# Optimization experiments

Hardware: AMD Instinct MI355X
Metric: run time of the kernel (lower is better)

The kernel has to match this reference:

```python
import jax, jax.numpy as jnp
import numpy as np

WS = 7          # window size (square)
HEADS = 16
LOGIT_MAX = float(np.log(1.0 / 0.01))


def _consts():
    # Continuous relative position bias coordinate table, Swin-v2 log-spaced.
    r = np.arange(-(WS - 1), WS)
    table = np.stack(np.meshgrid(r, r, indexing='ij'), axis=-1).astype(np.float32)  # [2W-1, 2W-1, 2]
    table = table / (WS - 1) * 8.0
    table = np.sign(table) * np.log2(np.abs(table) + 1.0) / np.log2(8.0)
    # Relative position index [N, N] into the flattened table.
    coords = np.stack(np.meshgrid(np.arange(WS), np.arange(WS), indexing='ij')).reshape(2, -1)
    rel = coords[:, :, None] - coords[:, None, :]
    idx = (rel[0] + WS - 1) * (2 * WS - 1) + (rel[1] + WS - 1)  # [49, 49]
    return table.reshape(-1, 2), idx.astype(np.int32)


def setup_inputs() -> dict:
    key = jax.random.key(0)
    ks = jax.random.split(key, 6)
    B, N, C = 2048, WS * WS, 512
    d = C // HEADS
    return {
        'x': jax.random.normal(ks[0], (B, N, C), jnp.float32),
        'w_qkv': jax.random.normal(ks[1], (C, 3 * C), jnp.float32) * (C ** -0.5),
        'q_bias': jnp.zeros((C,), jnp.float32),
        'v_bias': jnp.zeros((C,), jnp.float32),
        'logit_scale': jnp.full((HEADS, 1, 1), np.log(10.0), jnp.float32),
        'cpb_w1': jax.random.normal(ks[2], (2, 512), jnp.float32) * (2 ** -0.5),
        'cpb_b1': jnp.zeros((512,), jnp.float32),
        'cpb_w2': jax.random.normal(ks[3], (512, HEADS), jnp.float32) * (512 ** -0.5),
        'proj_w': jax.random.normal(ks[4], (C, C), jnp.float32) * (C ** -0.5),
        'proj_b': jnp.zeros((C,), jnp.float32),
    }


def _l2norm(x):
    # matches tf.math.l2_normalize (eps=1e-12 under a max)
    return x / jnp.sqrt(jnp.maximum(jnp.sum(x * x, axis=-1, keepdims=True), 1e-12))


def reference(x, w_qkv, q_bias, v_bias, logit_scale, cpb_w1, cpb_b1, cpb_w2, proj_w, proj_b):
    table, idx = _consts()
    table = jnp.asarray(table)   # [(2W-1)^2, 2]
    idx = jnp.asarray(idx)       # [N, N] int32 (constant)

    B, N, C = x.shape
    d = C // HEADS

    qkv = (x @ w_qkv).reshape(B, N, 3, HEADS, d).transpose(2, 0, 3, 1, 4)  # [3, B, H, N, d]
    q, k, v = qkv[0], qkv[1], qkv[2]
    q = q + q_bias.reshape(HEADS, 1, d)
    v = v + v_bias.reshape(HEADS, 1, d)

    # cosine attention with clamped learned logit scale
    attn = jnp.einsum('bhnd,bhmd->bhnm', _l2norm(q), _l2norm(k))
    scale = jnp.exp(jnp.minimum(logit_scale, LOGIT_MAX))  # [H,1,1]
    attn = attn * scale[None]

    # CPB MLP -> gather -> sigmoid bias
    bias_table = jax.nn.relu(table @ cpb_w1 + cpb_b1) @ cpb_w2          # [(2W-1)^2, H]
    bias = bias_table[idx.reshape(-1)].reshape(N, N, HEADS).transpose(2, 0, 1)  # [H, N, N]
    bias = 16.0 * jax.nn.sigmoid(bias)

    attn = jax.nn.softmax(attn + bias[None], axis=-1)

    out = jnp.einsum('bhnm,bhmd->bhnd', attn, v).transpose(0, 2, 1, 3).reshape(B, N, C)
    return out @ proj_w + proj_b
```

## Files before the change

### kernel.cpp

```cpp
#include <hip/hip_runtime.h>
#include <hip/hip_bf16.h>

typedef __bf16 bf16;
typedef __attribute__((ext_vector_type(8))) __bf16 bf16x8;
typedef __attribute__((ext_vector_type(4))) __bf16 bf16x4;
typedef __attribute__((ext_vector_type(4))) float floatx4;

#define HEADS 16
#define NTOK 49
#define MROWS (2048 * 49)
#define TILE_E 1568
#define LOGIT_MAX 4.6051702f


__device__ __forceinline__ void gload16(const void* g, void* l) {
  __builtin_amdgcn_global_load_lds((const __attribute__((address_space(1))) void*)g,
                                   (__attribute__((address_space(3))) void*)l, 16, 0, 0);
}


__global__ void cvt_x(const float* __restrict__ in, bf16* __restrict__ out, int n4) {
  int i = blockIdx.x * blockDim.x + threadIdx.x;
  const int stride = gridDim.x * blockDim.x;
  for (; i < n4; i += stride) {
    float4 v = ((const float4*)in)[i];
    bf16x4 o;
    o[0] = (bf16)v.x; o[1] = (bf16)v.y; o[2] = (bf16)v.z; o[3] = (bf16)v.w;
    *(bf16x4*)&out[(long)i * 4] = o;
  }
}

__global__ void transpose_bf16(const float* __restrict__ in, bf16* __restrict__ out,
                               int R, int C) {
  int idx = blockIdx.x * blockDim.x + threadIdx.x;
  if (idx < R * C) {
    int r = idx / C, c = idx % C;
    out[(long)c * R + r] = (bf16)in[(long)r * C + c];
  }
}


__global__ void cpb_mlp(const float* __restrict__ w1, const float* __restrict__ b1,
                        const float* __restrict__ w2, float* __restrict__ out169) {
  const int r = blockIdx.x;
  const int ti = r / 13, tj = r % 13;
  float v0 = (float)(ti - 6) * (8.0f / 6.0f);
  float v1 = (float)(tj - 6) * (8.0f / 6.0f);
  float s0 = (v0 > 0.f) ? 1.f : ((v0 < 0.f) ? -1.f : 0.f);
  float s1 = (v1 > 0.f) ? 1.f : ((v1 < 0.f) ? -1.f : 0.f);
  const float t0 = s0 * log2f(fabsf(v0) + 1.0f) * (1.0f / 3.0f);
  const float t1 = s1 * log2f(fabsf(v1) + 1.0f) * (1.0f / 3.0f);

  float acc[16];
#pragma unroll
  for (int h = 0; h < 16; ++h) acc[h] = 0.f;

  for (int c = threadIdx.x; c < 512; c += 64) {
    float hv = fmaxf(t0 * w1[c] + t1 * w1[512 + c] + b1[c], 0.f);
#pragma unroll
    for (int h = 0; h < 16; ++h) acc[h] += hv * w2[c * 16 + h];
  }
#pragma unroll
  for (int h = 0; h < 16; ++h) {
    float s = acc[h];
    for (int off = 32; off > 0; off >>= 1) s += __shfl_down(s, off);
    if (threadIdx.x == 0) out169[r * 16 + h] = s;
  }
}

__global__ void bias_expand(const float* __restrict__ out169, float* __restrict__ bias_sig) {
  int idx = blockIdx.x * blockDim.x + threadIdx.x;
  if (idx < 16 * 64 * 52) {
    int h = idx / 3328;
    int rem = idx % 3328;
    int q = rem / 52, k = rem % 52;
    float val = 0.f;
    if (q < 49 && k < 49) {
      int di = q / 7 - k / 7 + 6;
      int dj = q % 7 - k % 7 + 6;
      float v = out169[(di * 13 + dj) * 16 + h];
      val = 16.0f / (1.0f + expf(-v));
    }
    bias_sig[idx] = val;
  }
}


__device__ __forceinline__ void stage_tile(const bf16* __restrict__ G, int ldg,
                                           bf16* lds, int w, int lane) {
#pragma unroll
  for (int j = 0; j < 4; ++j) {
    const int rr = w * 32 + j * 8;
    const int row = rr + (lane >> 3);
    const int slot = (lane & 7) ^ (lane >> 3);
    gload16(G + (long)row * ldg + slot * 8, lds + rr * 64);
  }
}

template <int EPI>
__global__ __launch_bounds__(256, 4)
void gemm128(const bf16* __restrict__ A, const bf16* __restrict__ BT,
             void* __restrict__ Cout, const float* __restrict__ bias0,
             const float* __restrict__ bias1,
             bf16* __restrict__ Qp, bf16* __restrict__ Kp, bf16* __restrict__ Vp,
             int NT, int K, long N) {
  __shared__ bf16 AS[128][64];
  __shared__ bf16 BS[128][64];
  const int tid = threadIdx.x;
  const int lane = tid & 63, w = tid >> 6;
  const int l15 = lane & 15, g = lane >> 4;
  const int wm = w >> 1, wn = w & 1;

  int wg = blockIdx.x;
  wg = (wg & 7) * ((int)gridDim.x >> 3) + (wg >> 3);
  const long m0 = (long)(wg / NT) * 128;
  const long n0 = (long)(wg % NT) * 128;

  const bf16* Ab = A + m0 * K;
  const bf16* Bb = BT + n0 * K;

  floatx4 acc[4][4] = {};

  const int NKT = K >> 6;
  for (int kt = 0; kt < NKT; ++kt) {
    __syncthreads();
    stage_tile(Ab + kt * 64, K, &AS[0][0], w, lane);
    stage_tile(Bb + kt * 64, K, &BS[0][0], w, lane);
    __syncthreads();
#pragma unroll
    for (int t = 0; t < 2; ++t) {
      const int s = t * 4 + g;
      bf16x8 af[4], bfr[4];
#pragma unroll
      for (int m = 0; m < 4; ++m) {
        const int row = wm * 64 + m * 16 + l15;
        af[m] = *(const bf16x8*)&AS[row][(s ^ (row & 7)) * 8];
      }
#pragma unroll
      for (int n = 0; n < 4; ++n) {
        const int row = wn * 64 + n * 16 + l15;
        bfr[n] = *(const bf16x8*)&BS[row][(s ^ (row & 7)) * 8];
      }
#pragma unroll
      for (int m = 0; m < 4; ++m)
#pragma unroll
        for (int n = 0; n < 4; ++n)
          acc[m][n] = __builtin_amdgcn_mfma_f32_16x16x32_bf16(af[m], bfr[n], acc[m][n], 0, 0, 0);
    }
  }

  if (EPI == 0) {
    const int mat = (int)(n0 >> 9);
    bf16* const dst = (mat == 0) ? Qp : ((mat == 1) ? Kp : Vp);
    float badd4[4];
    unsigned off4[4];
#pragma unroll
    for (int n = 0; n < 4; ++n) {
      const int coln = (int)n0 + wn * 64 + n * 16;
      const int hh = (coln >> 5) & 15;
      const int d = (coln & 16) + l15;
      off4[n] = (unsigned)hh * TILE_E + d;
      badd4[n] = (mat == 0) ? bias0[coln + l15]
               : ((mat == 2) ? bias1[coln + l15 - 1024] : 0.0f);
    }
#pragma unroll
    for (int m = 0; m < 4; ++m) {
#pragma unroll
      for (int r = 0; r < 4; ++r) {
        const unsigned row = (unsigned)m0 + wm * 64 + m * 16 + g * 4 + r;
        const unsigned b = row / 49u;
        const unsigned nr = row - b * 49u;
        const unsigned ebase = b * (16u * TILE_E) + nr * 32u;
#pragma unroll
        for (int n = 0; n < 4; ++n)
          dst[ebase + off4[n]] = (bf16)(acc[m][n][r] + badd4[n]);
      }
    }
  } else {
#pragma unroll
    for (int m = 0; m < 4; ++m) {
#pragma unroll
      for (int n = 0; n < 4; ++n) {
        const long col = n0 + wn * 64 + n * 16 + l15;
        const float badd = bias0[col];
#pragma unroll
        for (int r = 0; r < 4; ++r) {
          const long row = m0 + wm * 64 + m * 16 + g * 4 + r;
          ((float*)Cout)[row * N + col] = acc[m][n][r] + badd;
        }
      }
    }
  }
}


__global__ __launch_bounds__(256)
void attn_mfma(const bf16* __restrict__ Qa, const bf16* __restrict__ Ka,
               const bf16* __restrict__ Va, const float* __restrict__ bias_sig,
               const float* __restrict__ logit_scale, bf16* __restrict__ aout) {
  __shared__ __align__(16) bf16 Vlds[4][2048];
  const int tid = threadIdx.x;
  const int wave = tid >> 6, lane = tid & 63;
  const int l15 = lane & 15, g = lane >> 4;
  const int bh = blockIdx.x * 4 + wave;
  const int h = bh & 15;
  const long tbase = (long)bh * TILE_E;
  const bf16* Qt = Qa + tbase;
  const bf16* Kt = Ka + tbase;
  const bf16* Vt = Va + tbase;
  bf16* VL = Vlds[wave];

#pragma unroll
  for (int j = 0; j < 4; ++j)
    gload16(Vt + j * 512 + lane * 8, VL + j * 512);

  bf16x8 kraw[4], qraw[4];
#pragma unroll
  for (int t = 0; t < 4; ++t)
    kraw[t] = *(const bf16x8*)(Kt + (t * 16 + l15) * 32 + g * 8);
#pragma unroll
  for (int t = 0; t < 4; ++t)
    qraw[t] = *(const bf16x8*)(Qt + (t * 16 + l15) * 32 + g * 8);

  const float scale = __expf(fminf(logit_scale[h], LOGIT_MAX));

  bf16x8 kf[4], qf[4];
#pragma unroll
  for (int t = 0; t < 4; ++t) {
    float fv[8], ss = 0.f;
#pragma unroll
    for (int j = 0; j < 8; ++j) { fv[j] = (float)kraw[t][j]; ss += fv[j] * fv[j]; }
    ss += __shfl_xor(ss, 16);
    ss += __shfl_xor(ss, 32);
    const float rk = rsqrtf(fmaxf(ss, 1e-12f));
#pragma unroll
    for (int j = 0; j < 8; ++j) kf[t][j] = (bf16)(fv[j] * rk);
  }
#pragma unroll
  for (int t = 0; t < 4; ++t) {
    float fv[8], ss = 0.f;
#pragma unroll
    for (int j = 0; j < 8; ++j) { fv[j] = (float)qraw[t][j]; ss += fv[j] * fv[j]; }
    ss += __shfl_xor(ss, 16);
    ss += __shfl_xor(ss, 32);
    const float rq = rsqrtf(fmaxf(ss, 1e-12f));
#pragma unroll
    for (int j = 0; j < 8; ++j) qf[t][j] = (bf16)(fv[j] * rq);
  }

  asm volatile("s_waitcnt vmcnt(0)" ::: "memory");
  __builtin_amdgcn_sched_barrier(0);
  bf16x8 vf[2][2];
#pragma unroll
  for (int dt = 0; dt < 2; ++dt)
#pragma unroll
    for (int t = 0; t < 2; ++t)
#pragma unroll
      for (int i = 0; i < 8; ++i) {
        const int kk = t * 32 + (i >> 2) * 16 + g * 4 + (i & 3);
        vf[dt][t][i] = VL[kk * 32 + dt * 16 + l15];
      }

  const floatx4 zero = {};

#pragma unroll
  for (int qt = 0; qt < 4; ++qt) {
    const int qrow = qt * 16 + l15;

    float4 b4[4];
#pragma unroll
    for (int kt = 0; kt < 4; ++kt)
      b4[kt] = *(const float4*)(bias_sig + h * 3328 + qrow * 52 + kt * 16 + g * 4);

    floatx4 st[4];
#pragma unroll
    for (int kt = 0; kt < 4; ++kt)
      st[kt] = __builtin_amdgcn_mfma_f32_16x16x32_bf16(kf[kt], qf[qt], zero, 0, 0, 0);

    float sv[4][4];
    float m = -1e30f;
#pragma unroll
    for (int kt = 0; kt < 4; ++kt)
#pragma unroll
      for (int r = 0; r < 4; ++r) {
        const int k = kt * 16 + g * 4 + r;
        const float s = (k < NTOK) ? st[kt][r] * scale + ((const float*)&b4[kt])[r] : -1e30f;
        sv[kt][r] = s;
        m = fmaxf(m, s);
      }
    m = fmaxf(m, __shfl_xor(m, 16));
    m = fmaxf(m, __shfl_xor(m, 32));
    float l = 0.f;
#pragma unroll
    for (int kt = 0; kt < 4; ++kt)
#pragma unroll
      for (int r = 0; r < 4; ++r) {
        const float p = __expf(sv[kt][r] - m);
        sv[kt][r] = p;
        l += p;
      }
    l += __shfl_xor(l, 16);
    l += __shfl_xor(l, 32);
    const float inv = 1.0f / l;

    bf16x8 pa[2];
#pragma unroll
    for (int t = 0; t < 2; ++t)
#pragma unroll
      for (int i = 0; i < 8; ++i)
        pa[t][i] = (bf16)(sv[2 * t + (i >> 2)][i & 3] * inv);

    floatx4 ot[2] = {};
#pragma unroll
    for (int dt = 0; dt < 2; ++dt)
#pragma unroll
      for (int t = 0; t < 2; ++t)
        ot[dt] = __builtin_amdgcn_mfma_f32_16x16x32_bf16(pa[t], vf[dt][t], ot[dt], 0, 0, 0);

#pragma unroll
    for (int dt = 0; dt < 2; ++dt)
#pragma unroll
      for (int r = 0; r < 4; ++r) {
        const int qg2 = qt * 16 + g * 4 + r;
        if (qg2 < NTOK)
          aout[((long)(bh >> 4) * NTOK + qg2) * 512 + h * 32 + dt * 16 + l15] =
              (bf16)ot[dt][r];
      }
  }
}


extern "C" void kernel_launch(void* const* d_in, const int* in_sizes, int n_in,
                              void* d_out, int out_size, void* d_ws, size_t ws_size,
                              hipStream_t stream) {
  (void)in_sizes; (void)n_in; (void)out_size; (void)ws_size;
  const float* x           = (const float*)d_in[0];
  const float* w_qkv       = (const float*)d_in[1];
  const float* q_bias      = (const float*)d_in[2];
  const float* v_bias      = (const float*)d_in[3];
  const float* logit_scale = (const float*)d_in[4];
  const float* cpb_w1      = (const float*)d_in[5];
  const float* cpb_b1      = (const float*)d_in[6];
  const float* cpb_w2      = (const float*)d_in[7];
  const float* proj_w      = (const float*)d_in[8];
  const float* proj_b      = (const float*)d_in[9];
  float* out = (float*)d_out;

  char* ws = (char*)d_ws;
  const size_t ARR_B  = 102760448;
  const size_t WQT_B  = 1572864;
  const size_t PJT_B  = 524288;
  const size_t T169_B = 10816;
  bf16*  Qa       = (bf16*)ws;
  bf16*  Ka       = (bf16*)(ws + ARR_B);
  bf16*  Va       = (bf16*)(ws + 2 * ARR_B);
  bf16*  xbf      = (bf16*)(ws + 3 * ARR_B);
  bf16*  wqkvT    = (bf16*)(ws + 4 * ARR_B);
  bf16*  projT    = (bf16*)(ws + 4 * ARR_B + WQT_B);
  float* tab169   = (float*)(ws + 4 * ARR_B + WQT_B + PJT_B);
  float* bias_sig = (float*)(ws + 4 * ARR_B + WQT_B + PJT_B + T169_B);

  cvt_x<<<2048, 256, 0, stream>>>(x, xbf, MROWS * 512 / 4);
  transpose_bf16<<<3072, 256, 0, stream>>>(w_qkv, wqkvT, 512, 1536);
  transpose_bf16<<<1024, 256, 0, stream>>>(proj_w, projT, 512, 512);
  cpb_mlp<<<169, 64, 0, stream>>>(cpb_w1, cpb_b1, cpb_w2, tab169);
  bias_expand<<<208, 256, 0, stream>>>(tab169, bias_sig);

  gemm128<0><<<784 * 12, 256, 0, stream>>>(xbf, wqkvT, nullptr, q_bias, v_bias,
                                           Qa, Ka, Va, 12, 512, 1536);
  attn_mfma<<<8192, 256, 0, stream>>>(Qa, Ka, Va, bias_sig, logit_scale, xbf);
  gemm128<1><<<784 * 4, 256, 0, stream>>>(xbf, projT, out, proj_b, nullptr,
                                          nullptr, nullptr, nullptr, 4, 512, 512);
}
```

Before: 498.6 us.

## Fuse fp32-to-bf16 input conversion into QKV GEMM and stage attention output in LDS

Removes the separate cvt_x pass: the QKV GEMM now loads the fp32 activations directly into registers, converts them to bf16 and writes them into the swizzled LDS tile, while the weights still use async global-to-LDS loads. This avoids writing and re-reading a bf16 copy of x, but each of the 12 N-tiles re-reads twice as many bytes of fp32 A, and the loads are now synchronous. The attention kernel also writes its per-head output into an LDS buffer first and then stores 16-byte vectors to global memory instead of scattered 2-byte stores.

Result: slower. 642.6 us (+28.9%).

```diff
diff --git a/kernel.cpp b/kernel.cpp
--- a/kernel.cpp
+++ b/kernel.cpp
@@ -16,18 +16,6 @@
 __device__ __forceinline__ void gload16(const void* g, void* l) {
   __builtin_amdgcn_global_load_lds((const __attribute__((address_space(1))) void*)g,
                                    (__attribute__((address_space(3))) void*)l, 16, 0, 0);
-}
-
-
-__global__ void cvt_x(const float* __restrict__ in, bf16* __restrict__ out, int n4) {
-  int i = blockIdx.x * blockDim.x + threadIdx.x;
-  const int stride = gridDim.x * blockDim.x;
-  for (; i < n4; i += stride) {
-    float4 v = ((const float4*)in)[i];
-    bf16x4 o;
-    o[0] = (bf16)v.x; o[1] = (bf16)v.y; o[2] = (bf16)v.z; o[3] = (bf16)v.w;
-    *(bf16x4*)&out[(long)i * 4] = o;
-  }
 }
 
 __global__ void transpose_bf16(const float* __restrict__ in, bf16* __restrict__ out,
@@ -99,7 +87,7 @@
 
 template <int EPI>
 __global__ __launch_bounds__(256, 4)
-void gemm128(const bf16* __restrict__ A, const bf16* __restrict__ BT,
+void gemm128(const void* __restrict__ Ain, const bf16* __restrict__ BT,
              void* __restrict__ Cout, const float* __restrict__ bias0,
              const float* __restrict__ bias1,
              bf16* __restrict__ Qp, bf16* __restrict__ Kp, bf16* __restrict__ Vp,
@@ -116,7 +104,8 @@
   const long m0 = (long)(wg / NT) * 128;
   const long n0 = (long)(wg % NT) * 128;
 
-  const bf16* Ab = A + m0 * K;
+  const float* Af = (const float*)Ain + m0 * K;
+  const bf16* Ab = (const bf16*)Ain + m0 * K;
   const bf16* Bb = BT + n0 * K;
 
   floatx4 acc[4][4] = {};
@@ -124,8 +113,27 @@
   const int NKT = K >> 6;
   for (int kt = 0; kt < NKT; ++kt) {
     __syncthreads();
-    stage_tile(Ab + kt * 64, K, &AS[0][0], w, lane);
-    stage_tile(Bb + kt * 64, K, &BS[0][0], w, lane);
+    if (EPI == 0) {
+      float4 areg[8];
+#pragma unroll
+      for (int j = 0; j < 8; ++j) {
+        const int row = w * 32 + j * 4 + (lane >> 4);
+        areg[j] = *(const float4*)(Af + (long)row * K + kt * 64 + (lane & 15) * 4);
+      }
+      stage_tile(Bb + kt * 64, K, &BS[0][0], w, lane);
+      const int s = (lane & 15) >> 1;
+#pragma unroll
+      for (int j = 0; j < 8; ++j) {
+        const int row = w * 32 + j * 4 + (lane >> 4);
+        bf16x4 o;
+        o[0] = (bf16)areg[j].x; o[1] = (bf16)areg[j].y;
+        o[2] = (bf16)areg[j].z; o[3] = (bf16)areg[j].w;
+        *(bf16x4*)&AS[row][(s ^ (row & 7)) * 8 + (lane & 1) * 4] = o;
+      }
+    } else {
+      stage_tile(Ab + kt * 64, K, &AS[0][0], w, lane);
+      stage_tile(Bb + kt * 64, K, &BS[0][0], w, lane);
+    }
     __syncthreads();
 #pragma unroll
     for (int t = 0; t < 2; ++t) {
@@ -321,11 +329,22 @@
     for (int dt = 0; dt < 2; ++dt)
 #pragma unroll
       for (int r = 0; r < 4; ++r) {
-        const int qg2 = qt * 16 + g * 4 + r;
-        if (qg2 < NTOK)
-          aout[((long)(bh >> 4) * NTOK + qg2) * 512 + h * 32 + dt * 16 + l15] =
-              (bf16)ot[dt][r];
-      }
+        const int q = qt * 16 + g * 4 + r;
+        if (q < NTOK) VL[q * 40 + dt * 16 + l15] = (bf16)ot[dt][r];
+      }
+  }
+
+  asm volatile("s_waitcnt lgkmcnt(0)" ::: "memory");
+  __builtin_amdgcn_sched_barrier(0);
+  const long obase = (long)(bh >> 4) * NTOK * 512 + h * 32;
+#pragma unroll
+  for (int j = 0; j < 4; ++j) {
+    const int c = lane + 64 * j;
+    if (c < 196) {
+      const int row = c >> 2, part = c & 3;
+      bf16x8 v = *(const bf16x8*)&VL[row * 40 + part * 8];
+      *(bf16x8*)(aout + obase + (long)row * 512 + part * 8) = v;
+    }
   }
 }
 
@@ -360,13 +379,12 @@
   float* tab169   = (float*)(ws + 4 * ARR_B + WQT_B + PJT_B);
   float* bias_sig = (float*)(ws + 4 * ARR_B + WQT_B + PJT_B + T169_B);
 
-  cvt_x<<<2048, 256, 0, stream>>>(x, xbf, MROWS * 512 / 4);
   transpose_bf16<<<3072, 256, 0, stream>>>(w_qkv, wqkvT, 512, 1536);
   transpose_bf16<<<1024, 256, 0, stream>>>(proj_w, projT, 512, 512);
   cpb_mlp<<<169, 64, 0, stream>>>(cpb_w1, cpb_b1, cpb_w2, tab169);
   bias_expand<<<208, 256, 0, stream>>>(tab169, bias_sig);
 
-  gemm128<0><<<784 * 12, 256, 0, stream>>>(xbf, wqkvT, nullptr, q_bias, v_bias,
+  gemm128<0><<<784 * 12, 256, 0, stream>>>(x, wqkvT, nullptr, q_bias, v_bias,
                                            Qa, Ka, Va, 12, 512, 1536);
   attn_mfma<<<8192, 256, 0, stream>>>(Qa, Ka, Va, bias_sig, logit_scale, xbf);
   gemm128<1><<<784 * 4, 256, 0, stream>>>(xbf, projT, out, proj_b, nullptr,
```
